# Kernel tuning notes

Hardware: AMD Instinct MI355X
Metric: run time of the kernel (lower is better)

Reference implementation:

```python
import jax, jax.numpy as jnp
import numpy as np

# --- fixed model configuration (from init_kwargs) ---
NX, NY, NU, NP = 8, 8, 2, 5
DELTA = 0.01
PHO, CP, AR, AB = 5.0, 6.0, 3.0, 3.0
KR, KB, TD, QR, QB = 2.5, 1.5, 300.0, 200.0, 200.0
CAF, TF = 6.0, 320.0
YMEAN = jnp.array([50.0, 1.0, 0.5, 313.0, 50.0, 1.0, 0.5, 313.0], jnp.float32)
YSTD = jnp.array([2.0, 0.2, 0.1, 4.0, 2.0, 0.2, 0.1, 4.0], jnp.float32)
UMEAN = jnp.array([10.0, 5.0], jnp.float32)
USTD = jnp.array([1.0, 0.5], jnp.float32)


def _fg(x, u):
    """Grey-box CSTR+flash ODE RHS. x: [B,8] scaled, u: [B,2] scaled."""
    x = x * YSTD + YMEAN
    u = u * USTD + UMEAN
    Hr, CAr, CBr, Tr = x[..., 0:1], x[..., 1:2], x[..., 2:3], x[..., 3:4]
    Hb, CAb, CBb, Tb = x[..., 4:5], x[..., 5:6], x[..., 6:7], x[..., 7:8]
    F, D = u[..., 0:1], u[..., 1:2]
    Fr = KR * jnp.sqrt(Hr)
    Fb = KB * jnp.sqrt(Hb)
    dHr = (F + D - Fr) / AR
    dCAr = (F * (CAF - CAr) - D * CAr) / (AR * Hr)
    dCBr = (-F * CBr - D * CBr) / (AR * Hr)
    dTr = (F * (TF - Tr) + D * (TD - Tr)) / (AR * Hr) + QR / (PHO * AR * CP * Hr)
    dHb = (Fr - Fb - D) / AB
    dCAb = (Fr * (CAr - CAb) + D * CAb) / (AB * Hb)
    dCBb = (Fr * (CBr - CBb) + D * CBb) / (AB * Hb)
    dTb = Fr * (Tr - Tb) / (AB * Hb) + QB / (PHO * AB * CP * Hb)
    xdot = jnp.concatenate([dHr, dCAr, dCBr, dTr, dHb, dCAb, dCBb, dTb], axis=-1)
    return xdot / YSTD


def setup_inputs() -> dict:
    key = jax.random.key(0)
    ks = jax.random.split(key, 6)
    B, T = 2048, 128
    d_in, d_h = NX + NP * (NY + NU) + NU, 128  # 60, 128
    useq = jax.random.normal(ks[0], (B, T, NU), jnp.float32)
    xGz0 = jax.random.normal(ks[1], (B, NX + NP * (NY + NU)), jnp.float32)
    W1 = jax.random.normal(ks[2], (d_in, d_h), jnp.float32) * (1.0 / np.sqrt(d_in))
    b1 = jnp.zeros((d_h,), jnp.float32)
    W2 = jax.random.normal(ks[3], (d_h, d_h), jnp.float32) * (1.0 / np.sqrt(d_h))
    b2 = jnp.zeros((d_h,), jnp.float32)
    W3 = jax.random.normal(ks[4], (d_h, NX), jnp.float32) * (1.0 / np.sqrt(d_h))
    b3 = jnp.zeros((NX,), jnp.float32)
    return {"useq": useq, "xGz0": xGz0, "W1": W1, "b1": b1,
            "W2": W2, "b2": b2, "W3": W3, "b3": b3}


def reference(useq, xGz0, W1, b1, W2, b2, W3, b3):
    def fnn(inp):
        h = jnp.tanh(inp @ W1 + b1)
        h = jnp.tanh(h @ W2 + b2)
        return h @ W3 + b3

    def interp(yfull):  # [B,(Np+1)*Ny] -> [B,Np*Ny]
        B = yfull.shape[0]
        y = yfull.reshape(B, NP + 1, NY)
        return (0.5 * (y[:, :-1] + y[:, 1:])).reshape(B, NP * NY)

    def step(xGz, u):
        xG = xGz[:, :NX]
        z = xGz[:, NX:]
        ypseq = z[:, :NP * NY]
        upseq = z[:, NP * NY:]
        # k1
        k1 = _fg(xG, u) + fnn(jnp.concatenate((xG, z, u), axis=-1))
        # interpolated half-step past sequence
        yp_interp = interp(jnp.concatenate((ypseq, xG), axis=-1))
        z_half = jnp.concatenate((yp_interp, upseq), axis=-1)
        x2 = xG + DELTA * (k1 / 2)
        k2 = _fg(x2, u) + fnn(jnp.concatenate((x2, z_half, u), axis=-1))
        x3 = xG + DELTA * (k2 / 2)
        k3 = _fg(x3, u) + fnn(jnp.concatenate((x3, z_half, u), axis=-1))
        yp_shift = jnp.concatenate((ypseq[:, NY:], xG), axis=-1)
        z_full = jnp.concatenate((yp_shift, upseq), axis=-1)
        x4 = xG + DELTA * k3
        k4 = _fg(x4, u) + fnn(jnp.concatenate((x4, z_full, u), axis=-1))
        y = xG
        xGplus = xG + (DELTA / 6) * (k1 + 2 * k2 + 2 * k3 + k4)
        zplus = jnp.concatenate((yp_shift, upseq[:, NU:], u), axis=-1)
        return jnp.concatenate((xGplus, zplus), axis=-1), y

    u_t = jnp.swapaxes(useq, 0, 1)  # [T,B,Nu]
    _, ys = jax.lax.scan(step, xGz0, u_t)  # ys: [T,B,Ny]
    return jnp.swapaxes(ys, 0, 1)  # [B,T,Ny]
```

## Files before the change

kernel.cpp:

```cpp
#include <hip/hip_runtime.h>
#include <math.h>

#define BLOCK 512
#define ROWS 8

typedef __attribute__((ext_vector_type(8))) short s16x8;
typedef __attribute__((ext_vector_type(4))) float f32x4;

static constexpr int O_H1   = 0;
static constexpr int O_SU   = 1088;
static constexpr int O_PP   = 3168;
static constexpr int O_PRIV = 3680;
static constexpr int PRIV_DW = 640;
static constexpr int LDSN   = O_PRIV + 8 * PRIV_DW;

static constexpr float SCL = 2.88539008177792681f;

__device__ __forceinline__ unsigned short f2bf(float f) {
  unsigned u = __float_as_uint(f);
  return (unsigned short)((u + 0x7fffu + ((u >> 16) & 1u)) >> 16);
}
__device__ __forceinline__ unsigned cvt_pk_bf16(float lo, float hi) {
  unsigned r;
  asm("v_cvt_pk_bf16_f32 %0, %1, %2" : "=v"(r) : "v"(lo), "v"(hi));
  return r;
}
__device__ __forceinline__ unsigned short bf1(float v) {
  return (unsigned short)cvt_pk_bf16(v, v);
}
__device__ __forceinline__ float tanh_ps(float y) {
  float e = __builtin_amdgcn_exp2f(y);
  return fmaf(-2.f, __builtin_amdgcn_rcpf(e + 1.f), 1.f);
}

#define MFMA16(A, B, C) __builtin_amdgcn_mfma_f32_16x16x32_bf16((A), (B), (C), 0, 0, 0)

#define LDS_BARRIER() do {                                   \
    asm volatile("s_waitcnt lgkmcnt(0)" ::: "memory");       \
    __builtin_amdgcn_s_barrier();                            \
    __builtin_amdgcn_sched_barrier(0);                       \
  } while (0)

extern "C" __global__ void __launch_bounds__(BLOCK, 1)
cstr_rk4_mfma11(const float* __restrict__ useq, const float* __restrict__ xGz0,
                const float* __restrict__ W1, const float* __restrict__ b1,
                const float* __restrict__ W2, const float* __restrict__ b2,
                const float* __restrict__ W3, const float* __restrict__ b3,
                float* __restrict__ out)
{
  extern __shared__ float smf[];
  unsigned short* h1h = (unsigned short*)(smf + O_H1);
  unsigned*       h1u = (unsigned*)(smf + O_H1);
  float* su = smf + O_SU;
  float* pp = smf + O_PP;

  const int tid  = threadIdx.x;
  const int w    = tid >> 6;
  const int l    = tid & 63;
  const int nn   = l & 15;
  const int hh   = l >> 4;
  const int r    = l >> 3;
  const int c    = l & 7;
  const int base = blockIdx.x * ROWS;

  float* wp_ = smf + O_PRIV + w * PRIV_DW;
  unsigned short* inhp = (unsigned short*)wp_;
  float* xmp = wp_ + 576;

  for (int i = tid; i < 8 * 260; i += BLOCK) {
    int row = i / 260, col = i % 260;
    su[i] = (col < 256) ? useq[(size_t)base * 256 + row * 256 + col] : 0.f;
  }
  for (int i = l; i < 16 * 72; i += 64) {
    int n_ = i / 72, k = i % 72;
    unsigned short v = 0;
    if (n_ < ROWS) {
      if (k < 58)      v = f2bf(xGz0[(size_t)(base + n_) * 58 + k]);
      else if (k < 60) v = f2bf(useq[(size_t)(base + n_) * 256 + (k - 58)]);
    }
    inhp[i] = v;
  }
  xmp[l] = xGz0[(size_t)(base + r) * 58 + c];

  const size_t rowb = (size_t)(base + r) * 58;
  float xg  = xGz0[rowb + c];
  float yp0 = xGz0[rowb + 8 + c],  yp1 = xGz0[rowb + 16 + c];
  float yp2 = xGz0[rowb + 24 + c], yp3 = xGz0[rowb + 32 + c];
  float yp4 = xGz0[rowb + 40 + c];
  float upA = xGz0[rowb + 48 + c];
  float upB = (c < 2) ? xGz0[rowb + 56 + c] : 0.f;
  float b3r = b3[c];
  float kacc = 0.f;

  const int j = 16 * w + nn;
  s16x8 a10, a11, a20, a21, a22, a23, a3h;
  #pragma unroll
  for (int i = 0; i < 8; ++i) {
    int k0 = 8 * hh + i, k1 = 32 + 8 * hh + i;
    a10[i] = (short)f2bf(SCL * W1[k0 * 128 + j]);
    a11[i] = (short)((k1 < 60) ? f2bf(SCL * W1[k1 * 128 + j]) : 0);
    a20[i] = (short)f2bf(SCL * W2[(     8 * hh + i) * 128 + j]);
    a21[i] = (short)f2bf(SCL * W2[(32 + 8 * hh + i) * 128 + j]);
    a22[i] = (short)f2bf(SCL * W2[(64 + 8 * hh + i) * 128 + j]);
    a23[i] = (short)f2bf(SCL * W2[(96 + 8 * hh + i) * 128 + j]);
    unsigned short z = 0;
    if (i < 4 && nn < 8) z = f2bf(W3[(16 * w + 4 * hh + i) * 8 + nn]);
    a3h[i] = (short)z;
  }
  const float4 bt1 = *(const float4*)(b1 + 16 * w + 4 * hh);
  const float4 bt2 = *(const float4*)(b2 + 16 * w + 4 * hh);
  const f32x4 cinit1 = {SCL * bt1.x, SCL * bt1.y, SCL * bt1.z, SCL * bt1.w};
  const f32x4 cinit2 = {SCL * bt2.x, SCL * bt2.y, SCL * bt2.z, SCL * bt2.w};
  const f32x4 zf = {0.f, 0.f, 0.f, 0.f};

  __syncthreads();

  #pragma unroll 1
  for (int t = 0; t < 128; ++t) {
    const float u0r = su[r * 260 + 2 * t];
    const float u1r = su[r * 260 + 2 * t + 1];
    if (w == 0) out[((size_t)(base + r) * 128 + t) * 8 + c] = xg;

    #pragma unroll
    for (int s = 0; s < 4; ++s) {
      {
        s16x8 bb0 = *(const s16x8*)(inhp + nn * 72 + 8 * hh);
        s16x8 bb1 = *(const s16x8*)(inhp + nn * 72 + 32 + 8 * hh);
        f32x4 c1a = MFMA16(a10, bb0, cinit1);
        f32x4 c1b = MFMA16(a11, bb1, zf);
        f32x4 c1 = c1a + c1b;
        float t0 = tanh_ps(c1[0]);
        float t1 = tanh_ps(c1[1]);
        float t2 = tanh_ps(c1[2]);
        float t3 = tanh_ps(c1[3]);
        uint2 pk; pk.x = cvt_pk_bf16(t0, t1); pk.y = cvt_pk_bf16(t2, t3);
        *(uint2*)(h1u + nn * 68 + 8 * w + 2 * hh) = pk;
      }
      LDS_BARRIER();

      {
        const unsigned short* h1row = h1h + nn * 136;
        s16x8 q0 = *(const s16x8*)(h1row +  0 + 8 * hh);
        s16x8 q1 = *(const s16x8*)(h1row + 32 + 8 * hh);
        s16x8 q2 = *(const s16x8*)(h1row + 64 + 8 * hh);
        s16x8 q3 = *(const s16x8*)(h1row + 96 + 8 * hh);
        f32x4 c2a = MFMA16(a20, q0, cinit2);
        f32x4 c2b = MFMA16(a21, q1, zf);
        c2a = MFMA16(a22, q2, c2a);
        c2b = MFMA16(a23, q3, c2b);
        f32x4 c2 = c2a + c2b;
        float t0 = tanh_ps(c2[0]);
        float t1 = tanh_ps(c2[1]);
        float t2 = tanh_ps(c2[2]);
        float t3 = tanh_ps(c2[3]);
        s16x8 bf3;
        ((unsigned*)&bf3)[0] = cvt_pk_bf16(t0, t1);
        ((unsigned*)&bf3)[1] = cvt_pk_bf16(t2, t3);
        ((unsigned*)&bf3)[2] = 0u;
        ((unsigned*)&bf3)[3] = 0u;
        f32x4 c3p = MFMA16(a3h, bf3, zf);
        if (nn < 8 && hh < 2)
          *(float4*)(pp + w * 64 + nn * 8 + 4 * hh) =
              make_float4(c3p[0], c3p[1], c3p[2], c3p[3]);
      }
      LDS_BARRIER();

      {
        if (s == 0) {
          inhp[r * 72 +  8 + c] = bf1(0.5f * (yp0 + yp1));
          inhp[r * 72 + 16 + c] = bf1(0.5f * (yp1 + yp2));
          inhp[r * 72 + 24 + c] = bf1(0.5f * (yp2 + yp3));
          inhp[r * 72 + 32 + c] = bf1(0.5f * (yp3 + yp4));
          inhp[r * 72 + 40 + c] = bf1(0.5f * (yp4 + xg));
        } else if (s == 2) {
          inhp[r * 72 +  8 + c] = bf1(yp1);
          inhp[r * 72 + 16 + c] = bf1(yp2);
          inhp[r * 72 + 24 + c] = bf1(yp3);
          inhp[r * 72 + 32 + c] = bf1(yp4);
          inhp[r * 72 + 40 + c] = bf1(xg);
          yp0 = yp1; yp1 = yp2; yp2 = yp3; yp3 = yp4; yp4 = xg;
        } else if (s == 3) {
          float tA = __shfl(upA, (l & 56) + ((c + 2) & 7));
          float tB = __shfl(upB, (l & 56) + ((c >= 6) ? (c - 6) : 0));
          float nu = (c < 6) ? tA : tB;
          upA = nu;
          inhp[r * 72 + 48 + c] = bf1(nu);
          if (c < 2) {
            float uv = (c == 0) ? u0r : u1r;
            upB = uv;
            inhp[r * 72 + 56 + c] = bf1(uv);
            if (t < 127)
              inhp[r * 72 + 58 + c] = bf1(su[r * 260 + 2 * (t + 1) + c]);
          }
        }

        float p0 = pp[0 * 64 + l], p1 = pp[1 * 64 + l];
        float p2 = pp[2 * 64 + l], p3 = pp[3 * 64 + l];
        float p4 = pp[4 * 64 + l], p5 = pp[5 * 64 + l];
        float p6 = pp[6 * 64 + l], p7 = pp[7 * 64 + l];
        float4 xa = *(const float4*)(xmp + r * 8);
        float4 xb = *(const float4*)(xmp + r * 8 + 4);

        float Hr  = fmaf(xa.x, 2.f, 50.f),  CAr = fmaf(xa.y, 0.2f, 1.f);
        float CBr = fmaf(xa.z, 0.1f, 0.5f), Tr  = fmaf(xa.w, 4.f, 313.f);
        float Hb  = fmaf(xb.x, 2.f, 50.f),  CAb = fmaf(xb.y, 0.2f, 1.f);
        float CBb = fmaf(xb.z, 0.1f, 0.5f), Tb  = fmaf(xb.w, 4.f, 313.f);
        float F = u0r + 10.f, D = fmaf(u1r, 0.5f, 5.f);
        float Fr = 2.5f * sqrtf(Hr), Fb = 1.5f * sqrtf(Hb);
        float rH = __builtin_amdgcn_rcpf(3.f * Hr);
        float rB = __builtin_amdgcn_rcpf(3.f * Hb);
        float k0 = (F + D - Fr) * (1.f / 6.f);
        float k1 = (F * (6.f - CAr) - D * CAr) * (5.f * rH);
        float k2 = (-(F + D) * CBr) * (10.f * rH);
        float k3 = (F * (320.f - Tr) + D * (300.f - Tr)) * (0.25f * rH) + (5.f / 3.f) * rH;
        float k4 = (Fr - Fb - D) * (1.f / 6.f);
        float k5 = (Fr * (CAr - CAb) + D * CAb) * (5.f * rB);
        float k6 = (Fr * (CBr - CBb) + D * CBb) * (10.f * rB);
        float k7 = Fr * (Tr - Tb) * (0.25f * rB) + (5.f / 3.f) * rB;
        float fgc = (c & 4) ? ((c & 2) ? ((c & 1) ? k7 : k6) : ((c & 1) ? k5 : k4))
                            : ((c & 2) ? ((c & 1) ? k3 : k2) : ((c & 1) ? k1 : k0));

        float nv = b3r + (((p0 + p1) + (p2 + p3)) + ((p4 + p5) + (p6 + p7)));
        float kv = fgc + nv;
        float cc;
        if (s == 0)      { kacc = kv;                  cc = fmaf(kv, 0.005f, xg); }
        else if (s == 1) { kacc = fmaf(kv, 2.f, kacc); cc = fmaf(kv, 0.005f, xg); }
        else if (s == 2) { kacc = fmaf(kv, 2.f, kacc); cc = fmaf(kv, 0.01f,  xg); }
        else             { xg = fmaf(kacc + kv, 0.01f / 6.f, xg); cc = xg; }
        xmp[r * 8 + c] = cc;
        inhp[r * 72 + c] = bf1(cc);
      }
    }
  }
}

extern "C" void kernel_launch(void* const* d_in, const int* in_sizes, int n_in,
                              void* d_out, int out_size, void* d_ws, size_t ws_size,
                              hipStream_t stream) {
  const float* useq = (const float*)d_in[0];
  const float* xGz0 = (const float*)d_in[1];
  const float* W1   = (const float*)d_in[2];
  const float* b1   = (const float*)d_in[3];
  const float* W2   = (const float*)d_in[4];
  const float* b2   = (const float*)d_in[5];
  const float* W3   = (const float*)d_in[6];
  const float* b3   = (const float*)d_in[7];
  float* out = (float*)d_out;

  size_t lds = (size_t)LDSN * sizeof(float);
  (void)hipFuncSetAttribute((const void*)cstr_rk4_mfma11,
                            hipFuncAttributeMaxDynamicSharedMemorySize, (int)lds);
  hipLaunchKernelGGL(cstr_rk4_mfma11, dim3(2048 / ROWS), dim3(BLOCK), lds, stream,
                     useq, xGz0, W1, b1, W2, b2, W3, b3, out);
}
```

Before: 493.0 us.

## Halve waves per block, each wave computing two 16-column hidden tiles

```diff
diff --git a/kernel.cpp b/kernel.cpp
--- a/kernel.cpp
+++ b/kernel.cpp
@@ -1,7 +1,7 @@
 #include <hip/hip_runtime.h>
 #include <math.h>
 
-#define BLOCK 512
+#define BLOCK 256
 #define ROWS 8
 
 typedef __attribute__((ext_vector_type(8))) short s16x8;
@@ -10,9 +10,9 @@
 static constexpr int O_H1   = 0;
 static constexpr int O_SU   = 1088;
 static constexpr int O_PP   = 3168;
-static constexpr int O_PRIV = 3680;
+static constexpr int O_PRIV = 3424;
 static constexpr int PRIV_DW = 640;
-static constexpr int LDSN   = O_PRIV + 8 * PRIV_DW;
+static constexpr int LDSN   = O_PRIV + 4 * PRIV_DW;
 
 static constexpr float SCL = 2.88539008177792681f;
 
@@ -42,7 +42,7 @@
   } while (0)
 
 extern "C" __global__ void __launch_bounds__(BLOCK, 1)
-cstr_rk4_mfma11(const float* __restrict__ useq, const float* __restrict__ xGz0,
+cstr_rk4_mfma12(const float* __restrict__ useq, const float* __restrict__ xGz0,
                 const float* __restrict__ W1, const float* __restrict__ b1,
                 const float* __restrict__ W2, const float* __restrict__ b2,
                 const float* __restrict__ W3, const float* __restrict__ b3,
@@ -92,25 +92,41 @@
   float b3r = b3[c];
   float kacc = 0.f;
 
-  const int j = 16 * w + nn;
-  s16x8 a10, a11, a20, a21, a22, a23, a3h;
+  const int j0 = 32 * w + nn;
+  const int j1 = 32 * w + 16 + nn;
+  s16x8 a10_0, a11_0, a10_1, a11_1;
+  s16x8 a20_0, a21_0, a22_0, a23_0, a20_1, a21_1, a22_1, a23_1;
+  s16x8 a3h_0, a3h_1;
   #pragma unroll
   for (int i = 0; i < 8; ++i) {
     int k0 = 8 * hh + i, k1 = 32 + 8 * hh + i;
-    a10[i] = (short)f2bf(SCL * W1[k0 * 128 + j]);
-    a11[i] = (short)((k1 < 60) ? f2bf(SCL * W1[k1 * 128 + j]) : 0);
-    a20[i] = (short)f2bf(SCL * W2[(     8 * hh + i) * 128 + j]);
-    a21[i] = (short)f2bf(SCL * W2[(32 + 8 * hh + i) * 128 + j]);
-    a22[i] = (short)f2bf(SCL * W2[(64 + 8 * hh + i) * 128 + j]);
-    a23[i] = (short)f2bf(SCL * W2[(96 + 8 * hh + i) * 128 + j]);
-    unsigned short z = 0;
-    if (i < 4 && nn < 8) z = f2bf(W3[(16 * w + 4 * hh + i) * 8 + nn]);
-    a3h[i] = (short)z;
-  }
-  const float4 bt1 = *(const float4*)(b1 + 16 * w + 4 * hh);
-  const float4 bt2 = *(const float4*)(b2 + 16 * w + 4 * hh);
-  const f32x4 cinit1 = {SCL * bt1.x, SCL * bt1.y, SCL * bt1.z, SCL * bt1.w};
-  const f32x4 cinit2 = {SCL * bt2.x, SCL * bt2.y, SCL * bt2.z, SCL * bt2.w};
+    a10_0[i] = (short)f2bf(SCL * W1[k0 * 128 + j0]);
+    a11_0[i] = (short)((k1 < 60) ? f2bf(SCL * W1[k1 * 128 + j0]) : 0);
+    a10_1[i] = (short)f2bf(SCL * W1[k0 * 128 + j1]);
+    a11_1[i] = (short)((k1 < 60) ? f2bf(SCL * W1[k1 * 128 + j1]) : 0);
+    a20_0[i] = (short)f2bf(SCL * W2[(     8 * hh + i) * 128 + j0]);
+    a21_0[i] = (short)f2bf(SCL * W2[(32 + 8 * hh + i) * 128 + j0]);
+    a22_0[i] = (short)f2bf(SCL * W2[(64 + 8 * hh + i) * 128 + j0]);
+    a23_0[i] = (short)f2bf(SCL * W2[(96 + 8 * hh + i) * 128 + j0]);
+    a20_1[i] = (short)f2bf(SCL * W2[(     8 * hh + i) * 128 + j1]);
+    a21_1[i] = (short)f2bf(SCL * W2[(32 + 8 * hh + i) * 128 + j1]);
+    a22_1[i] = (short)f2bf(SCL * W2[(64 + 8 * hh + i) * 128 + j1]);
+    a23_1[i] = (short)f2bf(SCL * W2[(96 + 8 * hh + i) * 128 + j1]);
+    unsigned short z0 = 0, z1 = 0;
+    if (i < 4 && nn < 8) {
+      z0 = f2bf(W3[(32 * w +      4 * hh + i) * 8 + nn]);
+      z1 = f2bf(W3[(32 * w + 16 + 4 * hh + i) * 8 + nn]);
+    }
+    a3h_0[i] = (short)z0; a3h_1[i] = (short)z1;
+  }
+  const float4 bt1_0 = *(const float4*)(b1 + 32 * w + 4 * hh);
+  const float4 bt1_1 = *(const float4*)(b1 + 32 * w + 16 + 4 * hh);
+  const float4 bt2_0 = *(const float4*)(b2 + 32 * w + 4 * hh);
+  const float4 bt2_1 = *(const float4*)(b2 + 32 * w + 16 + 4 * hh);
+  const f32x4 ci1_0 = {SCL * bt1_0.x, SCL * bt1_0.y, SCL * bt1_0.z, SCL * bt1_0.w};
+  const f32x4 ci1_1 = {SCL * bt1_1.x, SCL * bt1_1.y, SCL * bt1_1.z, SCL * bt1_1.w};
+  const f32x4 ci2_0 = {SCL * bt2_0.x, SCL * bt2_0.y, SCL * bt2_0.z, SCL * bt2_0.w};
+  const f32x4 ci2_1 = {SCL * bt2_1.x, SCL * bt2_1.y, SCL * bt2_1.z, SCL * bt2_1.w};
   const f32x4 zf = {0.f, 0.f, 0.f, 0.f};
 
   __syncthreads();
@@ -126,15 +142,19 @@
       {
         s16x8 bb0 = *(const s16x8*)(inhp + nn * 72 + 8 * hh);
         s16x8 bb1 = *(const s16x8*)(inhp + nn * 72 + 32 + 8 * hh);
-        f32x4 c1a = MFMA16(a10, bb0, cinit1);
-        f32x4 c1b = MFMA16(a11, bb1, zf);
-        f32x4 c1 = c1a + c1b;
-        float t0 = tanh_ps(c1[0]);
-        float t1 = tanh_ps(c1[1]);
-        float t2 = tanh_ps(c1[2]);
-        float t3 = tanh_ps(c1[3]);
-        uint2 pk; pk.x = cvt_pk_bf16(t0, t1); pk.y = cvt_pk_bf16(t2, t3);
-        *(uint2*)(h1u + nn * 68 + 8 * w + 2 * hh) = pk;
+        f32x4 c1a0 = MFMA16(a10_0, bb0, ci1_0);
+        f32x4 c1b0 = MFMA16(a11_0, bb1, zf);
+        f32x4 c1a1 = MFMA16(a10_1, bb0, ci1_1);
+        f32x4 c1b1 = MFMA16(a11_1, bb1, zf);
+        f32x4 c1_0 = c1a0 + c1b0;
+        f32x4 c1_1 = c1a1 + c1b1;
+        uint2 pk0, pk1;
+        pk0.x = cvt_pk_bf16(tanh_ps(c1_0[0]), tanh_ps(c1_0[1]));
+        pk0.y = cvt_pk_bf16(tanh_ps(c1_0[2]), tanh_ps(c1_0[3]));
+        pk1.x = cvt_pk_bf16(tanh_ps(c1_1[0]), tanh_ps(c1_1[1]));
+        pk1.y = cvt_pk_bf16(tanh_ps(c1_1[2]), tanh_ps(c1_1[3]));
+        *(uint2*)(h1u + nn * 68 + 8 * (2 * w)     + 2 * hh) = pk0;
+        *(uint2*)(h1u + nn * 68 + 8 * (2 * w + 1) + 2 * hh) = pk1;
       }
       LDS_BARRIER();
 
@@ -144,21 +164,27 @@
         s16x8 q1 = *(const s16x8*)(h1row + 32 + 8 * hh);
         s16x8 q2 = *(const s16x8*)(h1row + 64 + 8 * hh);
         s16x8 q3 = *(const s16x8*)(h1row + 96 + 8 * hh);
-        f32x4 c2a = MFMA16(a20, q0, cinit2);
-        f32x4 c2b = MFMA16(a21, q1, zf);
-        c2a = MFMA16(a22, q2, c2a);
-        c2b = MFMA16(a23, q3, c2b);
-        f32x4 c2 = c2a + c2b;
-        float t0 = tanh_ps(c2[0]);
-        float t1 = tanh_ps(c2[1]);
-        float t2 = tanh_ps(c2[2]);
-        float t3 = tanh_ps(c2[3]);
-        s16x8 bf3;
-        ((unsigned*)&bf3)[0] = cvt_pk_bf16(t0, t1);
-        ((unsigned*)&bf3)[1] = cvt_pk_bf16(t2, t3);
-        ((unsigned*)&bf3)[2] = 0u;
-        ((unsigned*)&bf3)[3] = 0u;
-        f32x4 c3p = MFMA16(a3h, bf3, zf);
+        f32x4 c2a0 = MFMA16(a20_0, q0, ci2_0);
+        f32x4 c2b0 = MFMA16(a21_0, q1, zf);
+        f32x4 c2a1 = MFMA16(a20_1, q0, ci2_1);
+        f32x4 c2b1 = MFMA16(a21_1, q1, zf);
+        c2a0 = MFMA16(a22_0, q2, c2a0);
+        c2b0 = MFMA16(a23_0, q3, c2b0);
+        c2a1 = MFMA16(a22_1, q2, c2a1);
+        c2b1 = MFMA16(a23_1, q3, c2b1);
+        f32x4 c2_0 = c2a0 + c2b0;
+        f32x4 c2_1 = c2a1 + c2b1;
+        s16x8 bf3a, bf3b;
+        ((unsigned*)&bf3a)[0] = cvt_pk_bf16(tanh_ps(c2_0[0]), tanh_ps(c2_0[1]));
+        ((unsigned*)&bf3a)[1] = cvt_pk_bf16(tanh_ps(c2_0[2]), tanh_ps(c2_0[3]));
+        ((unsigned*)&bf3a)[2] = 0u;
+        ((unsigned*)&bf3a)[3] = 0u;
+        ((unsigned*)&bf3b)[0] = cvt_pk_bf16(tanh_ps(c2_1[0]), tanh_ps(c2_1[1]));
+        ((unsigned*)&bf3b)[1] = cvt_pk_bf16(tanh_ps(c2_1[2]), tanh_ps(c2_1[3]));
+        ((unsigned*)&bf3b)[2] = 0u;
+        ((unsigned*)&bf3b)[3] = 0u;
+        f32x4 c3p = MFMA16(a3h_0, bf3a, zf);
+        c3p = MFMA16(a3h_1, bf3b, c3p);
         if (nn < 8 && hh < 2)
           *(float4*)(pp + w * 64 + nn * 8 + 4 * hh) =
               make_float4(c3p[0], c3p[1], c3p[2], c3p[3]);
@@ -196,8 +222,6 @@
 
         float p0 = pp[0 * 64 + l], p1 = pp[1 * 64 + l];
         float p2 = pp[2 * 64 + l], p3 = pp[3 * 64 + l];
-        float p4 = pp[4 * 64 + l], p5 = pp[5 * 64 + l];
-        float p6 = pp[6 * 64 + l], p7 = pp[7 * 64 + l];
         float4 xa = *(const float4*)(xmp + r * 8);
         float4 xb = *(const float4*)(xmp + r * 8 + 4);
 
@@ -220,7 +244,7 @@
         float fgc = (c & 4) ? ((c & 2) ? ((c & 1) ? k7 : k6) : ((c & 1) ? k5 : k4))
                             : ((c & 2) ? ((c & 1) ? k3 : k2) : ((c & 1) ? k1 : k0));
 
-        float nv = b3r + (((p0 + p1) + (p2 + p3)) + ((p4 + p5) + (p6 + p7)));
+        float nv = b3r + ((p0 + p1) + (p2 + p3));
         float kv = fgc + nv;
         float cc;
         if (s == 0)      { kacc = kv;                  cc = fmaf(kv, 0.005f, xg); }
@@ -248,8 +272,8 @@
   float* out = (float*)d_out;
 
   size_t lds = (size_t)LDSN * sizeof(float);
-  (void)hipFuncSetAttribute((const void*)cstr_rk4_mfma11,
+  (void)hipFuncSetAttribute((const void*)cstr_rk4_mfma12,
                             hipFuncAttributeMaxDynamicSharedMemorySize, (int)lds);
-  hipLaunchKernelGGL(cstr_rk4_mfma11, dim3(2048 / ROWS), dim3(BLOCK), lds, stream,
+  hipLaunchKernelGGL(cstr_rk4_mfma12, dim3(2048 / ROWS), dim3(BLOCK), lds, stream,
                      useq, xGz0, W1, b1, W2, b2, W3, b3, out);
 }
```

Result: slower. 535.8 us (+8.7%).
